# Optimization experiments

Hardware: AMD Instinct MI355X
Metric: run time of the kernel (lower is better)

Reference implementation:

```python
import jax, jax.numpy as jnp
import numpy as np

LAMBDA_CHAMFER = 1.0
LAMBDA_EDGE = 0.1


def setup_inputs() -> dict:
    key = jax.random.key(0)
    k1, k2, k3 = jax.random.split(key, 3)
    B, N, M, E = 8, 4096, 4096, 12288
    pred_vertices = jax.random.normal(k1, (B, N, 3), dtype=jnp.float32)
    gt_vertices = jax.random.normal(k2, (B, M, 3), dtype=jnp.float32)
    edges = jax.random.randint(k3, (E, 2), 0, N, dtype=jnp.int64)
    return {"pred_vertices": pred_vertices, "gt_vertices": gt_vertices, "edges": edges}


def _pairwise_dist(p1, p2):
    # ||x - y|| computed via the expanded form to avoid a [B,N,M,3] intermediate.
    # dist2[b,n,m] = |p1[b,n]|^2 + |p2[b,m]|^2 - 2 * p1[b,n] . p2[b,m]
    sq1 = jnp.sum(p1 * p1, axis=-1)  # [B, N]
    sq2 = jnp.sum(p2 * p2, axis=-1)  # [B, M]
    cross = jnp.einsum('bnd,bmd->bnm', p1, p2)  # [B, N, M]
    dist2 = sq1[:, :, None] + sq2[:, None, :] - 2.0 * cross
    return jnp.sqrt(jnp.maximum(dist2, 0.0))


def chamfer_distance(p1, p2):
    dist = _pairwise_dist(p1, p2)  # [B, N, M]
    min_p1 = jnp.min(dist, axis=2)  # [B, N] nearest gt for each pred point
    min_p2 = jnp.min(dist, axis=1)  # [B, M] nearest pred for each gt point
    return jnp.mean(min_p1) + jnp.mean(min_p2)


def edge_length_regularization(vertices, edges):
    v1 = vertices[:, edges[:, 0]]  # [B, E, 3]
    v2 = vertices[:, edges[:, 1]]  # [B, E, 3]
    lengths = jnp.linalg.norm(v1 - v2, axis=2)  # [B, E]
    return jnp.var(lengths, ddof=1)  # torch.var is unbiased by default


def reference(pred_vertices, gt_vertices, edges):
    cd = chamfer_distance(pred_vertices, gt_vertices)
    edge_loss = edge_length_regularization(pred_vertices, edges)
    return LAMBDA_CHAMFER * cd + LAMBDA_EDGE * edge_loss
```

## Files before the change

kernel.cpp:

```cpp
#include <hip/hip_runtime.h>
#include <hip/hip_bf16.h>
#include <float.h>

constexpr int B = 8, N = 4096, M = 4096, E = 12288;
constexpr int BLOCK = 256;
constexpr int VEC = 8;
constexpr int QPB = BLOCK * VEC;
constexpr int QT = N / QPB;
constexpr int RCH = 256;
constexpr int NRC = M / RCH;
constexpr int BLK_PER_DIR = B * QT * NRC;


__global__ void init_ws(unsigned* __restrict__ minbuf, float* __restrict__ acc) {
    int i = blockIdx.x * blockDim.x + threadIdx.x;
    const int total = 2 * B * N;
    for (; i < total; i += gridDim.x * blockDim.x) minbuf[i] = 0xFFFFFFFFu;
    if (blockIdx.x == 0 && threadIdx.x < 4) acc[threadIdx.x] = 0.0f;
}

__global__ __launch_bounds__(BLOCK) void chamfer_min_kernel(
    const float* __restrict__ pred, const float* __restrict__ gt,
    unsigned* __restrict__ minAll) {
    const int bid = blockIdx.x;
    const int dir = bid >> 8;
    const int r   = bid & (BLK_PER_DIR - 1);
    const int b   = r >> 5;
    const int rem = r & 31;
    const int qt  = rem >> 4;
    const int rc  = rem & 15;

    const float* __restrict__ q   = dir ? gt   : pred;
    const float* __restrict__ ref = dir ? pred : gt;
    unsigned* __restrict__ minOut = minAll + dir * (B * N);

    const int t = threadIdx.x;
    const int qbase = qt * QPB;

    float qx[VEC], qy[VEC], qz[VEC], h1[VEC];
#pragma unroll
    for (int i = 0; i < VEC; i++) {
        const int n = qbase + t + i * BLOCK;
        const float* p = q + ((size_t)b * N + n) * 3;
        qx[i] = p[0]; qy[i] = p[1]; qz[i] = p[2];
        h1[i] = 0.5f * (qx[i] * qx[i] + qy[i] * qy[i] + qz[i] * qz[i]);
    }

    __shared__ float4 tile[RCH];
    {
        const float* rp = ref + ((size_t)b * M + rc * RCH + t) * 3;
        float x = rp[0], y = rp[1], z = rp[2];
        tile[t] = make_float4(x, y, z, 0.5f * (x * x + y * y + z * z));
    }
    __syncthreads();

    float mins[VEC];
#pragma unroll
    for (int i = 0; i < VEC; i++) mins[i] = FLT_MAX;

#pragma unroll 4
    for (int m = 0; m < RCH; m++) {
        const float4 p = tile[m];
#pragma unroll
        for (int i = 0; i < VEC; i++) {
            float d = h1[i] + p.w;
            d = fmaf(-qx[i], p.x, d);
            d = fmaf(-qy[i], p.y, d);
            d = fmaf(-qz[i], p.z, d);
            mins[i] = fminf(mins[i], d);
        }
    }

#pragma unroll
    for (int i = 0; i < VEC; i++) {
        const int n = qbase + t + i * BLOCK;
        const unsigned u = __float_as_uint(fmaxf(mins[i], 0.0f));
        atomicMin(minOut + (size_t)b * N + n, u);
    }
}

__global__ void reduce_chamfer(const unsigned* __restrict__ minAll,
                               float* __restrict__ acc) {
    int i = blockIdx.x * blockDim.x + threadIdx.x;
    float s = 0.0f;
    const int total = 2 * B * N;
    for (; i < total; i += gridDim.x * blockDim.x) {
        const float h = __uint_as_float(minAll[i]);
        s += sqrtf(fmaxf(2.0f * h, 0.0f));
    }
#pragma unroll
    for (int o = 32; o > 0; o >>= 1) s += __shfl_down(s, o, 64);
    __shared__ float wsum[4];
    const int wave = threadIdx.x >> 6, lane = threadIdx.x & 63;
    if (lane == 0) wsum[wave] = s;
    __syncthreads();
    if (threadIdx.x == 0) {
        float tot = 0.0f;
        for (int w = 0; w < (int)(blockDim.x >> 6); w++) tot += wsum[w];
        atomicAdd(&acc[0], tot);
    }
}

__global__ void edge_kernel(const float* __restrict__ pred,
                            const int* __restrict__ edges,
                            float* __restrict__ acc) {
    const int j = blockIdx.x * blockDim.x + threadIdx.x;
    float L = 0.0f, L2 = 0.0f;
    if (j < B * E) {
        const int b = j / E, e = j - b * E;
        const int i0 = edges[2 * e], i1 = edges[2 * e + 1];
        const float* p0 = pred + ((size_t)b * N + i0) * 3;
        const float* p1 = pred + ((size_t)b * N + i1) * 3;
        const float dx = p0[0] - p1[0];
        const float dy = p0[1] - p1[1];
        const float dz = p0[2] - p1[2];
        L  = sqrtf(dx * dx + dy * dy + dz * dz);
        L2 = L * L;
    }
#pragma unroll
    for (int o = 32; o > 0; o >>= 1) {
        L  += __shfl_down(L, o, 64);
        L2 += __shfl_down(L2, o, 64);
    }
    __shared__ float w1[4], w2[4];
    const int wave = threadIdx.x >> 6, lane = threadIdx.x & 63;
    if (lane == 0) { w1[wave] = L; w2[wave] = L2; }
    __syncthreads();
    if (threadIdx.x == 0) {
        float a = 0.0f, c = 0.0f;
        for (int w = 0; w < 4; w++) { a += w1[w]; c += w2[w]; }
        atomicAdd(&acc[2], a);
        atomicAdd(&acc[3], c);
    }
}

__global__ void final_kernel(const float* __restrict__ acc,
                             float* __restrict__ out) {
    if (threadIdx.x == 0 && blockIdx.x == 0) {
        const float cd = acc[0] / 32768.0f;
        const float K = (float)(B * E);
        const float var = (acc[3] - acc[2] * acc[2] / K) / (K - 1.0f);
        out[0] = cd + 0.1f * var;
    }
}

extern "C" void kernel_launch(void* const* d_in, const int* in_sizes, int n_in,
                              void* d_out, int out_size, void* d_ws, size_t ws_size,
                              hipStream_t stream) {
    const float* pred  = (const float*)d_in[0];
    const float* gt    = (const float*)d_in[1];
    const int*   edges = (const int*)d_in[2];
    float* out = (float*)d_out;

    unsigned* minAll = (unsigned*)d_ws;
    float*    acc    = (float*)d_ws + 2 * B * N;

    init_ws<<<64, 256, 0, stream>>>(minAll, acc);
    chamfer_min_kernel<<<2 * BLK_PER_DIR, BLOCK, 0, stream>>>(pred, gt, minAll);
    edge_kernel<<<(B * E + BLOCK - 1) / BLOCK, BLOCK, 0, stream>>>(pred, edges, acc);
    reduce_chamfer<<<128, 256, 0, stream>>>(minAll, acc);
    final_kernel<<<1, 64, 0, stream>>>(acc, out);
}
```

Measured before the change: 102.4 us.

## Fuse chamfer and edge work into one kernel with full-reference scan per query

Each chamfer block now handles 256 queries with one query per thread and scans all reference points itself, using double-buffered shared tiles and prefetching the next chunk. Because each block sees every reference point, the atomicMin buffer, its init kernel and the separate reduce kernel are gone. Edge-length work runs in extra blocks of the same launch and writes per-block partial sums, which a single final kernel reduces deterministically. This removes several kernel launches and the atomics, but leaves only 256 chamfer blocks with lower per-thread reuse of each shared load, so occupancy and LDS bandwidth may limit it.

```diff
diff --git a/kernel.cpp b/kernel.cpp
--- a/kernel.cpp
+++ b/kernel.cpp
@@ -4,143 +4,160 @@
 
 constexpr int B = 8, N = 4096, M = 4096, E = 12288;
 constexpr int BLOCK = 256;
-constexpr int VEC = 8;
-constexpr int QPB = BLOCK * VEC;
-constexpr int QT = N / QPB;
-constexpr int RCH = 256;
-constexpr int NRC = M / RCH;
-constexpr int BLK_PER_DIR = B * QT * NRC;
+constexpr int CH = 512;
+constexpr int NCH = M / CH;
+constexpr int CHAM_BLOCKS = 2 * B * (N / BLOCK);
+constexpr int EDGE_BLOCKS = (B * E) / BLOCK;
+constexpr int EPB = (E / BLOCK);
 
 
-__global__ void init_ws(unsigned* __restrict__ minbuf, float* __restrict__ acc) {
-    int i = blockIdx.x * blockDim.x + threadIdx.x;
-    const int total = 2 * B * N;
-    for (; i < total; i += gridDim.x * blockDim.x) minbuf[i] = 0xFFFFFFFFu;
-    if (blockIdx.x == 0 && threadIdx.x < 4) acc[threadIdx.x] = 0.0f;
-}
+__global__ __launch_bounds__(BLOCK) void fused_kernel(
+    const float* __restrict__ pred, const float* __restrict__ gt,
+    const int* __restrict__ edges, float* __restrict__ ws) {
+    const int bid = blockIdx.x;
+    const int t = threadIdx.x;
 
-__global__ __launch_bounds__(BLOCK) void chamfer_min_kernel(
-    const float* __restrict__ pred, const float* __restrict__ gt,
-    unsigned* __restrict__ minAll) {
-    const int bid = blockIdx.x;
-    const int dir = bid >> 8;
-    const int r   = bid & (BLK_PER_DIR - 1);
-    const int b   = r >> 5;
-    const int rem = r & 31;
-    const int qt  = rem >> 4;
-    const int rc  = rem & 15;
+    if (bid < CHAM_BLOCKS) {
+        const int dir = bid >> 7;
+        const int b   = (bid >> 4) & 7;
+        const int qt  = bid & 15;
+        const float* __restrict__ q   = dir ? gt   : pred;
+        const float* __restrict__ ref = dir ? pred : gt;
 
-    const float* __restrict__ q   = dir ? gt   : pred;
-    const float* __restrict__ ref = dir ? pred : gt;
-    unsigned* __restrict__ minOut = minAll + dir * (B * N);
+        const float* qp = q + ((size_t)b * N + qt * BLOCK + t) * 3;
+        const float qx = qp[0], qy = qp[1], qz = qp[2];
+        const float h1 = 0.5f * (qx * qx + qy * qy + qz * qz);
 
-    const int t = threadIdx.x;
-    const int qbase = qt * QPB;
+        __shared__ float4 tile[2][CH];
+        const float2* rbase = (const float2*)(ref + (size_t)b * M * 3);
 
-    float qx[VEC], qy[VEC], qz[VEC], h1[VEC];
+        float2 r0 = rbase[3 * t], r1 = rbase[3 * t + 1], r2 = rbase[3 * t + 2];
+        {
+            const float x0 = r0.x, y0 = r0.y, z0 = r1.x;
+            const float x1 = r1.y, y1 = r2.x, z1 = r2.y;
+            tile[0][2 * t]     = make_float4(x0, y0, z0, 0.5f * (x0*x0 + y0*y0 + z0*z0));
+            tile[0][2 * t + 1] = make_float4(x1, y1, z1, 0.5f * (x1*x1 + y1*y1 + z1*z1));
+        }
+        __syncthreads();
+
+        float acc[8];
 #pragma unroll
-    for (int i = 0; i < VEC; i++) {
-        const int n = qbase + t + i * BLOCK;
-        const float* p = q + ((size_t)b * N + n) * 3;
-        qx[i] = p[0]; qy[i] = p[1]; qz[i] = p[2];
-        h1[i] = 0.5f * (qx[i] * qx[i] + qy[i] * qy[i] + qz[i] * qz[i]);
-    }
+        for (int i = 0; i < 8; i++) acc[i] = FLT_MAX;
 
-    __shared__ float4 tile[RCH];
-    {
-        const float* rp = ref + ((size_t)b * M + rc * RCH + t) * 3;
-        float x = rp[0], y = rp[1], z = rp[2];
-        tile[t] = make_float4(x, y, z, 0.5f * (x * x + y * y + z * z));
-    }
-    __syncthreads();
+        auto compute8 = [&](const float4* pp) {
+#pragma unroll
+            for (int i = 0; i < 8; ++i) {
+                const float4 p = pp[i];
+                float d = h1 + p.w;
+                d = fmaf(-qx, p.x, d);
+                d = fmaf(-qy, p.y, d);
+                d = fmaf(-qz, p.z, d);
+                acc[i] = fminf(acc[i], d);
+            }
+        };
+        auto load8 = [&](float4* dst, const float4* tl, int g) {
+#pragma unroll
+            for (int i = 0; i < 8; ++i) dst[i] = tl[g * 8 + i];
+        };
 
-    float mins[VEC];
+        for (int c = 0; c < NCH; ++c) {
+            if (c + 1 < NCH) {
+                const float2* nb = rbase + (size_t)(c + 1) * (CH * 3 / 2);
+                r0 = nb[3 * t]; r1 = nb[3 * t + 1]; r2 = nb[3 * t + 2];
+            }
+
+            const float4* tl = tile[c & 1];
+            float4 bufA[8], bufB[8];
+            load8(bufA, tl, 0);
+#pragma unroll 1
+            for (int g = 0; g < CH / 8 - 2; g += 2) {
+                load8(bufB, tl, g + 1);
+                compute8(bufA);
+                load8(bufA, tl, g + 2);
+                compute8(bufB);
+            }
+            load8(bufB, tl, CH / 8 - 1);
+            compute8(bufA);
+            compute8(bufB);
+
+            if (c + 1 < NCH) {
+                const int nb = (c + 1) & 1;
+                const float x0 = r0.x, y0 = r0.y, z0 = r1.x;
+                const float x1 = r1.y, y1 = r2.x, z1 = r2.y;
+                tile[nb][2 * t]     = make_float4(x0, y0, z0, 0.5f * (x0*x0 + y0*y0 + z0*z0));
+                tile[nb][2 * t + 1] = make_float4(x1, y1, z1, 0.5f * (x1*x1 + y1*y1 + z1*z1));
+            }
+            __syncthreads();
+        }
+
+        float m = acc[0];
 #pragma unroll
-    for (int i = 0; i < VEC; i++) mins[i] = FLT_MAX;
-
-#pragma unroll 4
-    for (int m = 0; m < RCH; m++) {
-        const float4 p = tile[m];
+        for (int i = 1; i < 8; i++) m = fminf(m, acc[i]);
+        float s = sqrtf(fmaxf(2.0f * m, 0.0f));
 #pragma unroll
-        for (int i = 0; i < VEC; i++) {
-            float d = h1[i] + p.w;
-            d = fmaf(-qx[i], p.x, d);
-            d = fmaf(-qy[i], p.y, d);
-            d = fmaf(-qz[i], p.z, d);
-            mins[i] = fminf(mins[i], d);
+        for (int o = 32; o > 0; o >>= 1) s += __shfl_down(s, o, 64);
+        __shared__ float wsum[4];
+        const int wave = t >> 6, lane = t & 63;
+        if (lane == 0) wsum[wave] = s;
+        __syncthreads();
+        if (t == 0) {
+            ws[bid] = wsum[0] + wsum[1] + wsum[2] + wsum[3];
         }
-    }
-
-#pragma unroll
-    for (int i = 0; i < VEC; i++) {
-        const int n = qbase + t + i * BLOCK;
-        const unsigned u = __float_as_uint(fmaxf(mins[i], 0.0f));
-        atomicMin(minOut + (size_t)b * N + n, u);
-    }
-}
-
-__global__ void reduce_chamfer(const unsigned* __restrict__ minAll,
-                               float* __restrict__ acc) {
-    int i = blockIdx.x * blockDim.x + threadIdx.x;
-    float s = 0.0f;
-    const int total = 2 * B * N;
-    for (; i < total; i += gridDim.x * blockDim.x) {
-        const float h = __uint_as_float(minAll[i]);
-        s += sqrtf(fmaxf(2.0f * h, 0.0f));
-    }
-#pragma unroll
-    for (int o = 32; o > 0; o >>= 1) s += __shfl_down(s, o, 64);
-    __shared__ float wsum[4];
-    const int wave = threadIdx.x >> 6, lane = threadIdx.x & 63;
-    if (lane == 0) wsum[wave] = s;
-    __syncthreads();
-    if (threadIdx.x == 0) {
-        float tot = 0.0f;
-        for (int w = 0; w < (int)(blockDim.x >> 6); w++) tot += wsum[w];
-        atomicAdd(&acc[0], tot);
-    }
-}
-
-__global__ void edge_kernel(const float* __restrict__ pred,
-                            const int* __restrict__ edges,
-                            float* __restrict__ acc) {
-    const int j = blockIdx.x * blockDim.x + threadIdx.x;
-    float L = 0.0f, L2 = 0.0f;
-    if (j < B * E) {
-        const int b = j / E, e = j - b * E;
+    } else {
+        const int eb = bid - CHAM_BLOCKS;
+        const int b  = eb / EPB;
+        const int e  = (eb - b * EPB) * BLOCK + t;
         const int i0 = edges[2 * e], i1 = edges[2 * e + 1];
         const float* p0 = pred + ((size_t)b * N + i0) * 3;
         const float* p1 = pred + ((size_t)b * N + i1) * 3;
         const float dx = p0[0] - p1[0];
         const float dy = p0[1] - p1[1];
         const float dz = p0[2] - p1[2];
-        L  = sqrtf(dx * dx + dy * dy + dz * dz);
-        L2 = L * L;
+        float L  = sqrtf(dx * dx + dy * dy + dz * dz);
+        float L2 = L * L;
+#pragma unroll
+        for (int o = 32; o > 0; o >>= 1) {
+            L  += __shfl_down(L, o, 64);
+            L2 += __shfl_down(L2, o, 64);
+        }
+        __shared__ float w1[4], w2[4];
+        const int wave = t >> 6, lane = t & 63;
+        if (lane == 0) { w1[wave] = L; w2[wave] = L2; }
+        __syncthreads();
+        if (t == 0) {
+            ws[CHAM_BLOCKS + 2 * eb]     = w1[0] + w1[1] + w1[2] + w1[3];
+            ws[CHAM_BLOCKS + 2 * eb + 1] = w2[0] + w2[1] + w2[2] + w2[3];
+        }
+    }
+}
+
+__global__ __launch_bounds__(256) void final_kernel(
+    const float* __restrict__ ws, float* __restrict__ out) {
+    const int t = threadIdx.x;
+    float sc = ws[t];
+    float s1 = ws[CHAM_BLOCKS + 2 * t];
+    float s2 = ws[CHAM_BLOCKS + 2 * t + 1];
+    if (t < EDGE_BLOCKS - 256) {
+        s1 += ws[CHAM_BLOCKS + 2 * (t + 256)];
+        s2 += ws[CHAM_BLOCKS + 2 * (t + 256) + 1];
     }
 #pragma unroll
     for (int o = 32; o > 0; o >>= 1) {
-        L  += __shfl_down(L, o, 64);
-        L2 += __shfl_down(L2, o, 64);
+        sc += __shfl_down(sc, o, 64);
+        s1 += __shfl_down(s1, o, 64);
+        s2 += __shfl_down(s2, o, 64);
     }
-    __shared__ float w1[4], w2[4];
-    const int wave = threadIdx.x >> 6, lane = threadIdx.x & 63;
-    if (lane == 0) { w1[wave] = L; w2[wave] = L2; }
+    __shared__ float w[3][4];
+    const int wave = t >> 6, lane = t & 63;
+    if (lane == 0) { w[0][wave] = sc; w[1][wave] = s1; w[2][wave] = s2; }
     __syncthreads();
-    if (threadIdx.x == 0) {
-        float a = 0.0f, c = 0.0f;
-        for (int w = 0; w < 4; w++) { a += w1[w]; c += w2[w]; }
-        atomicAdd(&acc[2], a);
-        atomicAdd(&acc[3], c);
-    }
-}
-
-__global__ void final_kernel(const float* __restrict__ acc,
-                             float* __restrict__ out) {
-    if (threadIdx.x == 0 && blockIdx.x == 0) {
-        const float cd = acc[0] / 32768.0f;
+    if (t == 0) {
+        float S = 0.0f, A = 0.0f, C = 0.0f;
+#pragma unroll
+        for (int i = 0; i < 4; i++) { S += w[0][i]; A += w[1][i]; C += w[2][i]; }
         const float K = (float)(B * E);
-        const float var = (acc[3] - acc[2] * acc[2] / K) / (K - 1.0f);
-        out[0] = cd + 0.1f * var;
+        const float var = (C - A * A / K) / (K - 1.0f);
+        out[0] = S / 32768.0f + 0.1f * var;
     }
 }
 
@@ -151,13 +168,8 @@
     const float* gt    = (const float*)d_in[1];
     const int*   edges = (const int*)d_in[2];
     float* out = (float*)d_out;
+    float* wsf = (float*)d_ws;
 
-    unsigned* minAll = (unsigned*)d_ws;
-    float*    acc    = (float*)d_ws + 2 * B * N;
-
-    init_ws<<<64, 256, 0, stream>>>(minAll, acc);
-    chamfer_min_kernel<<<2 * BLK_PER_DIR, BLOCK, 0, stream>>>(pred, gt, minAll);
-    edge_kernel<<<(B * E + BLOCK - 1) / BLOCK, BLOCK, 0, stream>>>(pred, edges, acc);
-    reduce_chamfer<<<128, 256, 0, stream>>>(minAll, acc);
-    final_kernel<<<1, 64, 0, stream>>>(acc, out);
+    fused_kernel<<<CHAM_BLOCKS + EDGE_BLOCKS, BLOCK, 0, stream>>>(pred, gt, edges, wsf);
+    final_kernel<<<1, 256, 0, stream>>>(wsf, out);
 }
```

Result: slower. 119.4 us (+16.6%).
